# Kernel optimization log

Hardware: AMD Instinct MI355X
Metric: run time of the kernel (lower is better)

The kernel has to match this reference:

```python
import jax, jax.numpy as jnp
import numpy as np

NUM_HEADS = 8
QWH, QWW = 8, 8
KWH, KWW = 8, 8

def _relative_position_index():
    # Swin-style relative position index, exactly as in build()
    ch, cw = np.arange(QWH), np.arange(QWW)
    cq = np.stack(np.meshgrid(ch, cw, indexing='ij')).reshape(2, -1)  # [2, qN]
    ch, cw = np.arange(KWH), np.arange(KWW)
    ck = np.stack(np.meshgrid(ch, cw, indexing='ij')).reshape(2, -1)  # [2, kN]
    rel = (cq[:, :, None] - ck[:, None, :]).transpose(1, 2, 0)        # [qN, kN, 2]
    rel[:, :, 0] += KWH - 1
    rel[:, :, 1] += KWW - 1
    rel[:, :, 0] *= QWW + KWW - 1
    return rel.sum(-1)  # [qN, kN] int

_REL_IDX = jnp.asarray(_relative_position_index())

def setup_inputs() -> dict:
    key = jax.random.key(0)
    k1, k2, k3, k4 = jax.random.split(key, 4)
    B, C = 2048, 256
    q = jax.random.normal(k1, (B, QWH, QWW, C), dtype=jnp.float32)
    k = jax.random.normal(k2, (B, KWH, KWW, C), dtype=jnp.float32)
    v = jax.random.normal(k3, (B, KWH, KWW, C), dtype=jnp.float32)
    num_elements = (QWH + KWH - 1) * (QWW + KWW - 1)  # 225
    bias_table = 0.02 * jax.random.truncated_normal(
        k4, -2.0, 2.0, (num_elements, NUM_HEADS), dtype=jnp.float32)
    return {"q": q, "k": k, "v": v, "bias_table": bias_table}

def reference(q, k, v, bias_table):
    B, qWh, qWw, C = q.shape
    _, kWh, kWw, _ = k.shape
    qN, kN = qWh * qWw, kWh * kWw
    H = NUM_HEADS
    d = C // H
    scale = d ** -0.5
    # [B, N, H, d] -> [B, H, N, d]
    qh = q.reshape(B, qN, H, d).transpose(0, 2, 1, 3) * scale
    kh = k.reshape(B, kN, H, d).transpose(0, 2, 1, 3)
    vh = v.reshape(B, kN, H, d).transpose(0, 2, 1, 3)
    attn = jnp.einsum('bhqd,bhkd->bhqk', qh, kh)
    # gather relative-position bias: [qN, kN, H] -> [1, H, qN, kN]
    bias = bias_table[_REL_IDX].transpose(2, 0, 1)[None]
    attn = jax.nn.softmax(attn + bias, axis=-1)
    # bhqk,bhkd -> bqhd then merge heads back to channels
    x = jnp.einsum('bhqk,bhkd->bqhd', attn, vh).reshape(B, qWh, qWw, C)
    return x, attn
```

## Files before the change

kernel.cpp:

```cpp
#include <hip/hip_runtime.h>


#define NUM_HEADS 8

typedef __attribute__((ext_vector_type(8))) short bf16x8;
typedef __attribute__((ext_vector_type(4))) float f32x4;

__device__ inline unsigned cvt_pk_bf16(float lo, float hi) {
    unsigned r;
    asm("v_cvt_pk_bf16_f32 %0, %1, %2" : "=v"(r) : "v"(lo), "v"(hi));
    return r;
}

__global__ __launch_bounds__(256) void spatial_attn_mfma(
    const float* __restrict__ q,
    const float* __restrict__ k,
    const float* __restrict__ v,
    const float* __restrict__ bias_table,
    float* __restrict__ x_out,
    float* __restrict__ attn_out)
{
    __shared__ short q_lds[64 * 32];
    __shared__ short k_lds[64 * 32];
    __shared__ short vt_lds[32 * 64];
    __shared__ short p_lds[64 * 64];
    __shared__ float bias_s[225];

    const int bh  = blockIdx.x;
    const int b   = bh >> 3;
    const int h   = bh & 7;
    const int tid = threadIdx.x;
    const int lane = tid & 63;
    const int w    = tid >> 6;

    constexpr float LOG2E  = 1.4426950408889634f;
    constexpr float SCALE2 = 0.17677669529663687f * 1.4426950408889634f;
    const size_t base = ((size_t)b * 64) * 256 + h * 32;

    #pragma unroll
    for (int it = 0; it < 2; ++it) {
        const int i   = tid + it * 256;
        const int r   = i >> 3;
        const int d4  = (i & 7) * 4;
        const size_t off = base + (size_t)r * 256 + d4;
        const f32x4 qv = *(const f32x4*)(q + off);
        const f32x4 kv = *(const f32x4*)(k + off);
        const f32x4 vv = *(const f32x4*)(v + off);

        const int u  = d4 >> 3;
        const int so = r * 32 + ((u ^ ((r >> 1) & 3)) << 3) + (d4 & 7);
        uint2 qb, kb;
        qb.x = cvt_pk_bf16(qv[0] * SCALE2, qv[1] * SCALE2);
        qb.y = cvt_pk_bf16(qv[2] * SCALE2, qv[3] * SCALE2);
        kb.x = cvt_pk_bf16(kv[0], kv[1]);
        kb.y = cvt_pk_bf16(kv[2], kv[3]);
        *(uint2*)(&q_lds[so]) = qb;
        *(uint2*)(&k_lds[so]) = kb;

        const unsigned vb0 = cvt_pk_bf16(vv[0], vv[1]);
        const unsigned vb1 = cvt_pk_bf16(vv[2], vv[3]);
        const short vs[4] = { (short)vb0, (short)(vb0 >> 16),
                              (short)vb1, (short)(vb1 >> 16) };
        const int ur = r >> 3, rl = r & 7;
        #pragma unroll
        for (int j = 0; j < 4; ++j) {
            const int c = d4 + j;
            vt_lds[c * 64 + ((ur ^ (c & 7)) << 3) + rl] = vs[j];
        }
    }
    for (int i = tid; i < 225; i += 256)
        bias_s[i] = bias_table[i * NUM_HEADS + h] * LOG2E;
    __syncthreads();

    const int lr = lane & 15;
    const int lg = lane >> 4;
    const int arow = 16 * w + lr;
    const bf16x8 a_frag =
        *(const bf16x8*)(&q_lds[arow * 32 + ((lg ^ ((arow >> 1) & 3)) << 3)]);

    const int crow_base = 16 * w + lg * 4;

    f32x4 acc[4];
    {
        const int lrh = lr >> 3, lrl = lr & 7;
        #pragma unroll
        for (int j = 0; j < 4; ++j) {
            const int e  = 4 * lg + j;
            const int bj = (2 * w + (e >> 3) - lrh + 7) * 15 + (e & 7) - lrl + 7;
            #pragma unroll
            for (int t = 0; t < 4; ++t) acc[t][j] = bias_s[bj - 30 * t];
        }
    }
    #pragma unroll
    for (int t = 0; t < 4; ++t) {
        const int krow = 16 * t + lr;
        const bf16x8 b_frag =
            *(const bf16x8*)(&k_lds[krow * 32 + ((lg ^ ((krow >> 1) & 3)) << 3)]);
        acc[t] = __builtin_amdgcn_mfma_f32_16x16x32_bf16(a_frag, b_frag, acc[t], 0, 0, 0);
    }

    const size_t attn_base = (size_t)bh * 64 * 64;
    #pragma unroll
    for (int j = 0; j < 4; ++j) {
        const int rr = crow_base + j;
        float e0 = __builtin_amdgcn_exp2f(acc[0][j]);
        float e1 = __builtin_amdgcn_exp2f(acc[1][j]);
        float e2 = __builtin_amdgcn_exp2f(acc[2][j]);
        float e3 = __builtin_amdgcn_exp2f(acc[3][j]);
        float s = (e0 + e1) + (e2 + e3);
        s += __shfl_xor(s, 1);
        s += __shfl_xor(s, 2);
        s += __shfl_xor(s, 4);
        s += __shfl_xor(s, 8);
        const float inv = __builtin_amdgcn_rcpf(s);
        e0 *= inv; e1 *= inv; e2 *= inv; e3 *= inv;

        float* arow_out = attn_out + attn_base + (size_t)rr * 64;
        arow_out[lr]      = e0;
        arow_out[16 + lr] = e1;
        arow_out[32 + lr] = e2;
        arow_out[48 + lr] = e3;

        const unsigned p01 = cvt_pk_bf16(e0, e1);
        const unsigned p23 = cvt_pk_bf16(e2, e3);
        const int rsw = rr & 7, rb = rr * 64, cl = lr & 7, ch = (lr >> 3);
        p_lds[rb + (((0 + ch) ^ rsw) << 3) + cl] = (short)p01;
        p_lds[rb + (((2 + ch) ^ rsw) << 3) + cl] = (short)(p01 >> 16);
        p_lds[rb + (((4 + ch) ^ rsw) << 3) + cl] = (short)p23;
        p_lds[rb + (((6 + ch) ^ rsw) << 3) + cl] = (short)(p23 >> 16);
    }

    f32x4 o[2] = {};
    const int prow = 16 * w + lr;
    #pragma unroll
    for (int s = 0; s < 2; ++s) {
        const int unit = s * 4 + lg;
        const bf16x8 pa =
            *(const bf16x8*)(&p_lds[prow * 64 + ((unit ^ (prow & 7)) << 3)]);
        #pragma unroll
        for (int t = 0; t < 2; ++t) {
            const int c = 16 * t + lr;
            const bf16x8 vb =
                *(const bf16x8*)(&vt_lds[c * 64 + ((unit ^ (c & 7)) << 3)]);
            o[t] = __builtin_amdgcn_mfma_f32_16x16x32_bf16(pa, vb, o[t], 0, 0, 0);
        }
    }

    #pragma unroll
    for (int t = 0; t < 2; ++t) {
        #pragma unroll
        for (int j = 0; j < 4; ++j) {
            const int rr = crow_base + j;
            x_out[base + (size_t)rr * 256 + 16 * t + lr] = o[t][j];
        }
    }
}

extern "C" void kernel_launch(void* const* d_in, const int* in_sizes, int n_in,
                              void* d_out, int out_size, void* d_ws, size_t ws_size,
                              hipStream_t stream) {
    const float* q    = (const float*)d_in[0];
    const float* k    = (const float*)d_in[1];
    const float* v    = (const float*)d_in[2];
    const float* bias = (const float*)d_in[3];

    const int B = in_sizes[0] / (8 * 8 * 256);
    float* x_out    = (float*)d_out;
    float* attn_out = x_out + (size_t)B * 64 * 256;

    spatial_attn_mfma<<<dim3(B * NUM_HEADS), dim3(256), 0, stream>>>(
        q, k, v, bias, x_out, attn_out);
}
```

Measured before the change: 168.4 us.

## Make blocks persistent over 16 batch-head tiles with register prefetch of next tile

Each block now loops over 16 (batch, head) tiles, two batches by eight heads, and launches B/2 blocks instead of B*8. Global loads of q, k, v and the bias for the next tile go into registers while the current tile runs its MFMA and softmax. The Q fragment is loaded directly into MFMA A-operand layout, which drops the q LDS staging. This is meant to hide global load latency and amortize launch overhead, at the cost of extra registers, two barriers per tile and a launch_bounds occupancy hint.

```diff
diff --git a/kernel.cpp b/kernel.cpp
--- a/kernel.cpp
+++ b/kernel.cpp
@@ -4,6 +4,7 @@
 #define NUM_HEADS 8
 
 typedef __attribute__((ext_vector_type(8))) short bf16x8;
+typedef __attribute__((ext_vector_type(4))) unsigned u32x4;
 typedef __attribute__((ext_vector_type(4))) float f32x4;
 
 __device__ inline unsigned cvt_pk_bf16(float lo, float hi) {
@@ -12,7 +13,7 @@
     return r;
 }
 
-__global__ __launch_bounds__(256) void spatial_attn_mfma(
+__global__ __launch_bounds__(256, 4) void spatial_attn_mfma(
     const float* __restrict__ q,
     const float* __restrict__ k,
     const float* __restrict__ v,
@@ -20,138 +21,168 @@
     float* __restrict__ x_out,
     float* __restrict__ attn_out)
 {
-    __shared__ short q_lds[64 * 32];
     __shared__ short k_lds[64 * 32];
     __shared__ short vt_lds[32 * 64];
     __shared__ short p_lds[64 * 64];
     __shared__ float bias_s[225];
 
-    const int bh  = blockIdx.x;
-    const int b   = bh >> 3;
-    const int h   = bh & 7;
-    const int tid = threadIdx.x;
+    const int blk  = blockIdx.x;
+    const int tid  = threadIdx.x;
     const int lane = tid & 63;
     const int w    = tid >> 6;
+    const int lr   = lane & 15;
+    const int lg   = lane >> 4;
 
     constexpr float LOG2E  = 1.4426950408889634f;
     constexpr float SCALE2 = 0.17677669529663687f * 1.4426950408889634f;
-    const size_t base = ((size_t)b * 64) * 256 + h * 32;
-
-    #pragma unroll
-    for (int it = 0; it < 2; ++it) {
-        const int i   = tid + it * 256;
-        const int r   = i >> 3;
-        const int d4  = (i & 7) * 4;
-        const size_t off = base + (size_t)r * 256 + d4;
-        const f32x4 qv = *(const f32x4*)(q + off);
-        const f32x4 kv = *(const f32x4*)(k + off);
-        const f32x4 vv = *(const f32x4*)(v + off);
-
-        const int u  = d4 >> 3;
-        const int so = r * 32 + ((u ^ ((r >> 1) & 3)) << 3) + (d4 & 7);
-        uint2 qb, kb;
-        qb.x = cvt_pk_bf16(qv[0] * SCALE2, qv[1] * SCALE2);
-        qb.y = cvt_pk_bf16(qv[2] * SCALE2, qv[3] * SCALE2);
-        kb.x = cvt_pk_bf16(kv[0], kv[1]);
-        kb.y = cvt_pk_bf16(kv[2], kv[3]);
-        *(uint2*)(&q_lds[so]) = qb;
-        *(uint2*)(&k_lds[so]) = kb;
-
-        const unsigned vb0 = cvt_pk_bf16(vv[0], vv[1]);
-        const unsigned vb1 = cvt_pk_bf16(vv[2], vv[3]);
-        const short vs[4] = { (short)vb0, (short)(vb0 >> 16),
-                              (short)vb1, (short)(vb1 >> 16) };
-        const int ur = r >> 3, rl = r & 7;
-        #pragma unroll
-        for (int j = 0; j < 4; ++j) {
-            const int c = d4 + j;
-            vt_lds[c * 64 + ((ur ^ (c & 7)) << 3) + rl] = vs[j];
-        }
-    }
-    for (int i = tid; i < 225; i += 256)
-        bias_s[i] = bias_table[i * NUM_HEADS + h] * LOG2E;
-    __syncthreads();
-
-    const int lr = lane & 15;
-    const int lg = lane >> 4;
-    const int arow = 16 * w + lr;
-    const bf16x8 a_frag =
-        *(const bf16x8*)(&q_lds[arow * 32 + ((lg ^ ((arow >> 1) & 3)) << 3)]);
-
-    const int crow_base = 16 * w + lg * 4;
-
-    f32x4 acc[4];
-    {
-        const int lrh = lr >> 3, lrl = lr & 7;
-        #pragma unroll
-        for (int j = 0; j < 4; ++j) {
-            const int e  = 4 * lg + j;
-            const int bj = (2 * w + (e >> 3) - lrh + 7) * 15 + (e & 7) - lrl + 7;
+
+    const int r0   = tid >> 3;
+    const int d4   = (tid & 7) * 4;
+    const int qrow = 16 * w + lr;
+
+    f32x4 kr0, kr1, vr0, vr1, qr0, qr1;
+    float br = 0.f;
+
+    auto issue = [&](int tn) {
+        const int bb = 2 * blk + (tn >> 3);
+        const int hh = tn & 7;
+        const size_t bs = ((size_t)bb * 64) * 256 + hh * 32;
+        qr0 = *(const f32x4*)(q + bs + (size_t)qrow * 256 + 8 * lg);
+        qr1 = *(const f32x4*)(q + bs + (size_t)qrow * 256 + 8 * lg + 4);
+        kr0 = *(const f32x4*)(k + bs + (size_t)r0 * 256 + d4);
+        kr1 = *(const f32x4*)(k + bs + (size_t)(r0 + 32) * 256 + d4);
+        vr0 = *(const f32x4*)(v + bs + (size_t)r0 * 256 + d4);
+        vr1 = *(const f32x4*)(v + bs + (size_t)(r0 + 32) * 256 + d4);
+        if (tid < 225) br = bias_table[tid * NUM_HEADS + hh];
+    };
+
+    issue(0);
+
+    for (int t = 0; t < 16; ++t) {
+        const int b = 2 * blk + (t >> 3);
+        const int h = t & 7;
+        const size_t base      = ((size_t)b * 64) * 256 + h * 32;
+        const size_t attn_base = ((size_t)(b * NUM_HEADS + h)) * 64 * 64;
+
+        __syncthreads();
+
+        const int u = d4 >> 3;
+        {
+            const int rr = r0;
+            const int so = rr * 32 + ((u ^ ((rr >> 1) & 3)) << 3) + (d4 & 7);
+            uint2 kb;
+            kb.x = cvt_pk_bf16(kr0[0], kr0[1]);
+            kb.y = cvt_pk_bf16(kr0[2], kr0[3]);
+            *(uint2*)(&k_lds[so]) = kb;
+            const unsigned vb0 = cvt_pk_bf16(vr0[0], vr0[1]);
+            const unsigned vb1 = cvt_pk_bf16(vr0[2], vr0[3]);
+            const int ur = rr >> 3, rl = rr & 7;
+            vt_lds[(d4+0)*64 + ((ur ^ ((d4+0)&7)) << 3) + rl] = (short)vb0;
+            vt_lds[(d4+1)*64 + ((ur ^ ((d4+1)&7)) << 3) + rl] = (short)(vb0 >> 16);
+            vt_lds[(d4+2)*64 + ((ur ^ ((d4+2)&7)) << 3) + rl] = (short)vb1;
+            vt_lds[(d4+3)*64 + ((ur ^ ((d4+3)&7)) << 3) + rl] = (short)(vb1 >> 16);
+        }
+        {
+            const int rr = r0 + 32;
+            const int so = rr * 32 + ((u ^ ((rr >> 1) & 3)) << 3) + (d4 & 7);
+            uint2 kb;
+            kb.x = cvt_pk_bf16(kr1[0], kr1[1]);
+            kb.y = cvt_pk_bf16(kr1[2], kr1[3]);
+            *(uint2*)(&k_lds[so]) = kb;
+            const unsigned vb0 = cvt_pk_bf16(vr1[0], vr1[1]);
+            const unsigned vb1 = cvt_pk_bf16(vr1[2], vr1[3]);
+            const int ur = rr >> 3, rl = rr & 7;
+            vt_lds[(d4+0)*64 + ((ur ^ ((d4+0)&7)) << 3) + rl] = (short)vb0;
+            vt_lds[(d4+1)*64 + ((ur ^ ((d4+1)&7)) << 3) + rl] = (short)(vb0 >> 16);
+            vt_lds[(d4+2)*64 + ((ur ^ ((d4+2)&7)) << 3) + rl] = (short)vb1;
+            vt_lds[(d4+3)*64 + ((ur ^ ((d4+3)&7)) << 3) + rl] = (short)(vb1 >> 16);
+        }
+        if (tid < 225) bias_s[tid] = br * LOG2E;
+
+        u32x4 afu;
+        afu[0] = cvt_pk_bf16(qr0[0] * SCALE2, qr0[1] * SCALE2);
+        afu[1] = cvt_pk_bf16(qr0[2] * SCALE2, qr0[3] * SCALE2);
+        afu[2] = cvt_pk_bf16(qr1[0] * SCALE2, qr1[1] * SCALE2);
+        afu[3] = cvt_pk_bf16(qr1[2] * SCALE2, qr1[3] * SCALE2);
+        const bf16x8 a_frag = __builtin_bit_cast(bf16x8, afu);
+
+        __syncthreads();
+
+        if (t < 15) issue(t + 1);
+
+        const int crow_base = 16 * w + lg * 4;
+        f32x4 acc[4];
+        {
+            const int lrh = lr >> 3, lrl = lr & 7;
             #pragma unroll
-            for (int t = 0; t < 4; ++t) acc[t][j] = bias_s[bj - 30 * t];
-        }
-    }
-    #pragma unroll
-    for (int t = 0; t < 4; ++t) {
-        const int krow = 16 * t + lr;
-        const bf16x8 b_frag =
-            *(const bf16x8*)(&k_lds[krow * 32 + ((lg ^ ((krow >> 1) & 3)) << 3)]);
-        acc[t] = __builtin_amdgcn_mfma_f32_16x16x32_bf16(a_frag, b_frag, acc[t], 0, 0, 0);
-    }
-
-    const size_t attn_base = (size_t)bh * 64 * 64;
-    #pragma unroll
-    for (int j = 0; j < 4; ++j) {
-        const int rr = crow_base + j;
-        float e0 = __builtin_amdgcn_exp2f(acc[0][j]);
-        float e1 = __builtin_amdgcn_exp2f(acc[1][j]);
-        float e2 = __builtin_amdgcn_exp2f(acc[2][j]);
-        float e3 = __builtin_amdgcn_exp2f(acc[3][j]);
-        float s = (e0 + e1) + (e2 + e3);
-        s += __shfl_xor(s, 1);
-        s += __shfl_xor(s, 2);
-        s += __shfl_xor(s, 4);
-        s += __shfl_xor(s, 8);
-        const float inv = __builtin_amdgcn_rcpf(s);
-        e0 *= inv; e1 *= inv; e2 *= inv; e3 *= inv;
-
-        float* arow_out = attn_out + attn_base + (size_t)rr * 64;
-        arow_out[lr]      = e0;
-        arow_out[16 + lr] = e1;
-        arow_out[32 + lr] = e2;
-        arow_out[48 + lr] = e3;
-
-        const unsigned p01 = cvt_pk_bf16(e0, e1);
-        const unsigned p23 = cvt_pk_bf16(e2, e3);
-        const int rsw = rr & 7, rb = rr * 64, cl = lr & 7, ch = (lr >> 3);
-        p_lds[rb + (((0 + ch) ^ rsw) << 3) + cl] = (short)p01;
-        p_lds[rb + (((2 + ch) ^ rsw) << 3) + cl] = (short)(p01 >> 16);
-        p_lds[rb + (((4 + ch) ^ rsw) << 3) + cl] = (short)p23;
-        p_lds[rb + (((6 + ch) ^ rsw) << 3) + cl] = (short)(p23 >> 16);
-    }
-
-    f32x4 o[2] = {};
-    const int prow = 16 * w + lr;
-    #pragma unroll
-    for (int s = 0; s < 2; ++s) {
-        const int unit = s * 4 + lg;
-        const bf16x8 pa =
-            *(const bf16x8*)(&p_lds[prow * 64 + ((unit ^ (prow & 7)) << 3)]);
-        #pragma unroll
-        for (int t = 0; t < 2; ++t) {
-            const int c = 16 * t + lr;
-            const bf16x8 vb =
-                *(const bf16x8*)(&vt_lds[c * 64 + ((unit ^ (c & 7)) << 3)]);
-            o[t] = __builtin_amdgcn_mfma_f32_16x16x32_bf16(pa, vb, o[t], 0, 0, 0);
-        }
-    }
-
-    #pragma unroll
-    for (int t = 0; t < 2; ++t) {
+            for (int j = 0; j < 4; ++j) {
+                const int e  = 4 * lg + j;
+                const int bj = (2 * w + (e >> 3) - lrh + 7) * 15 + (e & 7) - lrl + 7;
+                #pragma unroll
+                for (int tt = 0; tt < 4; ++tt) acc[tt][j] = bias_s[bj - 30 * tt];
+            }
+        }
+        #pragma unroll
+        for (int tt = 0; tt < 4; ++tt) {
+            const int krow = 16 * tt + lr;
+            const bf16x8 b_frag =
+                *(const bf16x8*)(&k_lds[krow * 32 + ((lg ^ ((krow >> 1) & 3)) << 3)]);
+            acc[tt] = __builtin_amdgcn_mfma_f32_16x16x32_bf16(a_frag, b_frag, acc[tt], 0, 0, 0);
+        }
+
         #pragma unroll
         for (int j = 0; j < 4; ++j) {
             const int rr = crow_base + j;
-            x_out[base + (size_t)rr * 256 + 16 * t + lr] = o[t][j];
+            float e0 = __builtin_amdgcn_exp2f(acc[0][j]);
+            float e1 = __builtin_amdgcn_exp2f(acc[1][j]);
+            float e2 = __builtin_amdgcn_exp2f(acc[2][j]);
+            float e3 = __builtin_amdgcn_exp2f(acc[3][j]);
+            float s = (e0 + e1) + (e2 + e3);
+            s += __shfl_xor(s, 1);
+            s += __shfl_xor(s, 2);
+            s += __shfl_xor(s, 4);
+            s += __shfl_xor(s, 8);
+            const float inv = __builtin_amdgcn_rcpf(s);
+            e0 *= inv; e1 *= inv; e2 *= inv; e3 *= inv;
+
+            float* arow_out = attn_out + attn_base + (size_t)rr * 64;
+            arow_out[lr]      = e0;
+            arow_out[16 + lr] = e1;
+            arow_out[32 + lr] = e2;
+            arow_out[48 + lr] = e3;
+
+            const unsigned p01 = cvt_pk_bf16(e0, e1);
+            const unsigned p23 = cvt_pk_bf16(e2, e3);
+            const int rsw = rr & 7, rb = rr * 64, cl = lr & 7, ch = (lr >> 3);
+            p_lds[rb + (((0 + ch) ^ rsw) << 3) + cl] = (short)p01;
+            p_lds[rb + (((2 + ch) ^ rsw) << 3) + cl] = (short)(p01 >> 16);
+            p_lds[rb + (((4 + ch) ^ rsw) << 3) + cl] = (short)p23;
+            p_lds[rb + (((6 + ch) ^ rsw) << 3) + cl] = (short)(p23 >> 16);
+        }
+
+        f32x4 o[2] = {};
+        const int prow = 16 * w + lr;
+        #pragma unroll
+        for (int s = 0; s < 2; ++s) {
+            const int unit = s * 4 + lg;
+            const bf16x8 pa =
+                *(const bf16x8*)(&p_lds[prow * 64 + ((unit ^ (prow & 7)) << 3)]);
+            #pragma unroll
+            for (int tt = 0; tt < 2; ++tt) {
+                const int c = 16 * tt + lr;
+                const bf16x8 vb =
+                    *(const bf16x8*)(&vt_lds[c * 64 + ((unit ^ (c & 7)) << 3)]);
+                o[tt] = __builtin_amdgcn_mfma_f32_16x16x32_bf16(pa, vb, o[tt], 0, 0, 0);
+            }
+        }
+
+        #pragma unroll
+        for (int tt = 0; tt < 2; ++tt) {
+            #pragma unroll
+            for (int j = 0; j < 4; ++j) {
+                const int rr = crow_base + j;
+                x_out[base + (size_t)rr * 256 + 16 * tt + lr] = o[tt][j];
+            }
         }
     }
 }
@@ -168,6 +199,6 @@
     float* x_out    = (float*)d_out;
     float* attn_out = x_out + (size_t)B * 64 * 256;
 
-    spatial_attn_mfma<<<dim3(B * NUM_HEADS), dim3(256), 0, stream>>>(
+    spatial_attn_mfma<<<dim3(B / 2), dim3(256), 0, stream>>>(
         q, k, v, bias, x_out, attn_out);
 }
```

Result: no change. 168.0 us (-0.2%).

## Stage attn and x outputs through LDS for vectorized nontemporal stores

Applied to the files above, without the earlier changes.

Probabilities and the output tile are first written into a rotated shared-memory buffer. They are then read back as float4 rows and written to global memory with 16-byte nontemporal stores, replacing scattered scalar stores. The q/k/v loads also become nontemporal. The goal is better write coalescing on the store-bound attn output. The cost is 16 KB of extra LDS per block, which may lower occupancy. Each wave reuses its own attn_lds rows for x without a barrier, which relies on the earlier reads in that wave having completed.

```diff
diff --git a/kernel.cpp b/kernel.cpp
--- a/kernel.cpp
+++ b/kernel.cpp
@@ -24,6 +24,7 @@
     __shared__ short k_lds[64 * 32];
     __shared__ short vt_lds[32 * 64];
     __shared__ short p_lds[64 * 64];
+    __shared__ float attn_lds[64 * 64];
     __shared__ float bias_s[225];
 
     const int bh  = blockIdx.x;
@@ -43,9 +44,9 @@
         const int r   = i >> 3;
         const int d4  = (i & 7) * 4;
         const size_t off = base + (size_t)r * 256 + d4;
-        const f32x4 qv = *(const f32x4*)(q + off);
-        const f32x4 kv = *(const f32x4*)(k + off);
-        const f32x4 vv = *(const f32x4*)(v + off);
+        const f32x4 qv = __builtin_nontemporal_load((const f32x4*)(q + off));
+        const f32x4 kv = __builtin_nontemporal_load((const f32x4*)(k + off));
+        const f32x4 vv = __builtin_nontemporal_load((const f32x4*)(v + off));
 
         const int u  = d4 >> 3;
         const int so = r * 32 + ((u ^ ((r >> 1) & 3)) << 3) + (d4 & 7);
@@ -59,14 +60,11 @@
 
         const unsigned vb0 = cvt_pk_bf16(vv[0], vv[1]);
         const unsigned vb1 = cvt_pk_bf16(vv[2], vv[3]);
-        const short vs[4] = { (short)vb0, (short)(vb0 >> 16),
-                              (short)vb1, (short)(vb1 >> 16) };
         const int ur = r >> 3, rl = r & 7;
-        #pragma unroll
-        for (int j = 0; j < 4; ++j) {
-            const int c = d4 + j;
-            vt_lds[c * 64 + ((ur ^ (c & 7)) << 3) + rl] = vs[j];
-        }
+        vt_lds[(d4+0)*64 + ((ur ^ ((d4+0)&7)) << 3) + rl] = (short)vb0;
+        vt_lds[(d4+1)*64 + ((ur ^ ((d4+1)&7)) << 3) + rl] = (short)(vb0 >> 16);
+        vt_lds[(d4+2)*64 + ((ur ^ ((d4+2)&7)) << 3) + rl] = (short)vb1;
+        vt_lds[(d4+3)*64 + ((ur ^ ((d4+3)&7)) << 3) + rl] = (short)(vb1 >> 16);
     }
     for (int i = tid; i < 225; i += 256)
         bias_s[i] = bias_table[i * NUM_HEADS + h] * LOG2E;
@@ -99,7 +97,6 @@
         acc[t] = __builtin_amdgcn_mfma_f32_16x16x32_bf16(a_frag, b_frag, acc[t], 0, 0, 0);
     }
 
-    const size_t attn_base = (size_t)bh * 64 * 64;
     #pragma unroll
     for (int j = 0; j < 4; ++j) {
         const int rr = crow_base + j;
@@ -115,11 +112,11 @@
         const float inv = __builtin_amdgcn_rcpf(s);
         e0 *= inv; e1 *= inv; e2 *= inv; e3 *= inv;
 
-        float* arow_out = attn_out + attn_base + (size_t)rr * 64;
-        arow_out[lr]      = e0;
-        arow_out[16 + lr] = e1;
-        arow_out[32 + lr] = e2;
-        arow_out[48 + lr] = e3;
+        const int rb64 = rr * 64, rot = 4 * rr;
+        attn_lds[rb64 + ((lr      + rot) & 63)] = e0;
+        attn_lds[rb64 + ((16 + lr + rot) & 63)] = e1;
+        attn_lds[rb64 + ((32 + lr + rot) & 63)] = e2;
+        attn_lds[rb64 + ((48 + lr + rot) & 63)] = e3;
 
         const unsigned p01 = cvt_pk_bf16(e0, e1);
         const unsigned p23 = cvt_pk_bf16(e2, e3);
@@ -128,6 +125,16 @@
         p_lds[rb + (((2 + ch) ^ rsw) << 3) + cl] = (short)(p01 >> 16);
         p_lds[rb + (((4 + ch) ^ rsw) << 3) + cl] = (short)p23;
         p_lds[rb + (((6 + ch) ^ rsw) << 3) + cl] = (short)(p23 >> 16);
+    }
+
+    const size_t attn_base = (size_t)bh * 64 * 64;
+    #pragma unroll
+    for (int j2 = 0; j2 < 4; ++j2) {
+        const int rr = 16 * w + 4 * j2 + (lane >> 4);
+        const int c0 = 4 * (lane & 15);
+        const f32x4 av = *(const f32x4*)(&attn_lds[rr * 64 + ((c0 + 4 * rr) & 63)]);
+        __builtin_nontemporal_store(av,
+            (f32x4*)(attn_out + attn_base + (size_t)rr * 64 + c0));
     }
 
     f32x4 o[2] = {};
@@ -146,12 +153,23 @@
         }
     }
 
-    #pragma unroll
-    for (int t = 0; t < 2; ++t) {
+    {
+        float* xs = attn_lds + 16 * w * 64;
         #pragma unroll
-        for (int j = 0; j < 4; ++j) {
-            const int rr = crow_base + j;
-            x_out[base + (size_t)rr * 256 + 16 * t + lr] = o[t][j];
+        for (int t = 0; t < 2; ++t) {
+            #pragma unroll
+            for (int j = 0; j < 4; ++j) {
+                const int rr = crow_base + j;
+                xs[(rr & 15) * 32 + ((16 * t + lr + 4 * rr) & 31)] = o[t][j];
+            }
+        }
+        #pragma unroll
+        for (int j3 = 0; j3 < 2; ++j3) {
+            const int rr = 16 * w + 8 * j3 + (lane >> 3);
+            const int c0 = 4 * (lane & 7);
+            const f32x4 xv = *(const f32x4*)(&xs[(rr & 15) * 32 + ((c0 + 4 * rr) & 31)]);
+            __builtin_nontemporal_store(xv,
+                (f32x4*)(x_out + base + (size_t)rr * 256 + c0));
         }
     }
 }
```

After: 159.9 us. 5.0% less time.
